# Kernel optimization log

Hardware: AMD Instinct MI355X
Metric: run time of the kernel (lower is better)

The kernel has to match this reference:

```python
import jax, jax.numpy as jnp
import numpy as np

NEG_INF = -9e15  # matches torch's -9000000000000000.0 mask fill
LEAKY_SLOPE = 0.01  # F.leaky_relu default


def setup_inputs() -> dict:
    key = jax.random.key(0)
    ks = jax.random.split(key, 6)
    B, N, F_in, F_out = 4, 4096, 256, 128
    h = jax.random.normal(ks[0], (B, N, F_in), dtype=jnp.float32)
    adj = jax.random.randint(ks[1], (B, N, N), 0, 2, dtype=jnp.int32)
    W_w = jax.random.normal(ks[2], (F_out, F_in), dtype=jnp.float32) * (1.0 / np.sqrt(F_in))
    W_b = jax.random.normal(ks[3], (F_out,), dtype=jnp.float32) * 0.01
    a_w = jax.random.normal(ks[4], (2 * F_out,), dtype=jnp.float32) * (1.0 / np.sqrt(2 * F_out))
    a_b = jax.random.normal(ks[5], (), dtype=jnp.float32) * 0.01
    return {"h": h, "adj": adj, "W_w": W_w, "W_b": W_b, "a_w": a_w, "a_b": a_b}


def reference(h, adj, W_w, W_b, a_w, a_b):
    # Wh: [B, N, F_out]
    Wh = jnp.einsum('bnf,of->bno', h, W_w) + W_b
    F_out = Wh.shape[-1]
    # a([Wh_i, Wh_j]) decomposes as a_src.Wh_i + a_dst.Wh_j + a_b (linearity),
    # avoiding the O(N^2 * 2F) repeat+cat intermediate while computing identical math.
    a_src, a_dst = a_w[:F_out], a_w[F_out:]
    src = jnp.einsum('bno,o->bn', Wh, a_src)  # [B, N]
    dst = jnp.einsum('bno,o->bn', Wh, a_dst)  # [B, N]
    e = src[:, :, None] + dst[:, None, :] + a_b  # [B, N, N]
    e = jnp.where(e >= 0, e, LEAKY_SLOPE * e)  # leaky_relu
    masked = jnp.where(adj > 0, e, NEG_INF)
    attention = jax.nn.softmax(masked, axis=-1)  # row softmax over neighbors j
    h_prime = jnp.einsum('bij,bjo->bio', attention, Wh)
    return h_prime
```

## Files before the change

### kernel.cpp

```cpp
#include <hip/hip_runtime.h>
#include <hip/hip_bf16.h>

typedef __attribute__((ext_vector_type(4))) float f32x4;
typedef __attribute__((ext_vector_type(8))) short s16x8;
typedef unsigned long long u64;

#define NB_ 4
#define N_ 4096
#define FI_ 256
#define FO_ 128
#define NROWS 16384
#define SPLIT 4
#define JSTEP 32
#define NSTEPS ((N_ / SPLIT) / JSTEP)

__device__ __forceinline__ unsigned pkbf(float a, float b) {
    __hip_bfloat162 t = __float22bfloat162_rn(make_float2(a, b));
    unsigned r; __builtin_memcpy(&r, &t, 4); return r;
}

typedef __attribute__((address_space(1))) const void CGV;
typedef __attribute__((address_space(3))) void LDSV;
__device__ __forceinline__ void gload16(const void* g, void* l) {
    __builtin_amdgcn_global_load_lds((CGV*)g, (LDSV*)l, 16, 0, 0);
}

__global__ __launch_bounds__(256) void k0_packw(
    const float* __restrict__ Ww, __hip_bfloat16* __restrict__ whi,
    __hip_bfloat16* __restrict__ wlo)
{
    int idx = blockIdx.x * 256 + threadIdx.x;
    float v = Ww[idx];
    __hip_bfloat16 hi = __float2bfloat16(v);
    whi[idx] = hi;
    wlo[idx] = __float2bfloat16(v - __bfloat162float(hi));
}

__global__ __launch_bounds__(256) void k1_wh(
    const float* __restrict__ h, const __hip_bfloat16* __restrict__ whi,
    const __hip_bfloat16* __restrict__ wlo, const float* __restrict__ Wb,
    const float* __restrict__ aw, const float* __restrict__ ab,
    __hip_bfloat16* __restrict__ WhT, float* __restrict__ srcv,
    float* __restrict__ dstbv, unsigned* __restrict__ auxp)
{
    __shared__ float lds[16][132];
    const int tid = threadIdx.x;
    const int w = tid >> 6, l = tid & 63;
    const int lr = l & 15, g = l >> 4;
    const int r0 = blockIdx.x * 16;
    const float* hp = h + (size_t)(r0 + lr) * FI_ + g * 8;

    f32x4 acc[2] = {(f32x4)0.f, (f32x4)0.f};

    #pragma unroll
    for (int kt = 0; kt < 8; ++kt) {
        f32x4 x0 = *(const f32x4*)(hp + kt * 32);
        f32x4 x1 = *(const f32x4*)(hp + kt * 32 + 4);
        float xx[8];
        #pragma unroll
        for (int t = 0; t < 4; ++t) { xx[t] = x0[t]; xx[t + 4] = x1[t]; }
        union { s16x8 v; unsigned u[4]; } ahi, alo;
        #pragma unroll
        for (int t = 0; t < 4; ++t) {
            float a0 = xx[2 * t], a1 = xx[2 * t + 1];
            unsigned uh = pkbf(a0, a1);
            ahi.u[t] = uh;
            float h0f = __uint_as_float(uh << 16);
            float h1f = __uint_as_float(uh & 0xffff0000u);
            alo.u[t] = pkbf(a0 - h0f, a1 - h1f);
        }
        #pragma unroll
        for (int c = 0; c < 2; ++c) {
            const int o = w * 32 + c * 16 + lr;
            s16x8 bh = *(const s16x8*)(whi + (size_t)o * FI_ + kt * 32 + g * 8);
            s16x8 bl = *(const s16x8*)(wlo + (size_t)o * FI_ + kt * 32 + g * 8);
            acc[c] = __builtin_amdgcn_mfma_f32_16x16x32_bf16(ahi.v, bh, acc[c], 0, 0, 0);
            acc[c] = __builtin_amdgcn_mfma_f32_16x16x32_bf16(alo.v, bh, acc[c], 0, 0, 0);
            acc[c] = __builtin_amdgcn_mfma_f32_16x16x32_bf16(ahi.v, bl, acc[c], 0, 0, 0);
        }
    }

    #pragma unroll
    for (int c = 0; c < 2; ++c) {
        int col = w * 32 + c * 16 + lr;
        float wb = Wb[col];
        #pragma unroll
        for (int kk = 0; kk < 4; ++kk)
            lds[g * 4 + kk][col] = acc[c][kk] + wb;
    }
    __syncthreads();

    {
        const int o = tid >> 1, half = tid & 1;
        const int bb = r0 >> 12, nn = (r0 & 4095) + half * 8;
        union { s16x8 v; unsigned u[4]; } af;
        #pragma unroll
        for (int i = 0; i < 4; ++i)
            af.u[i] = pkbf(lds[half * 8 + 2 * i][o], lds[half * 8 + 2 * i + 1][o]);
        *(s16x8*)(WhT + ((size_t)bb * FO_ + o) * N_ + nn) = af.v;
    }

    {
        const int row = tid >> 4, seg = tid & 15;
        float sp = 0.f, dp = 0.f;
        #pragma unroll
        for (int i = 0; i < 8; ++i) {
            float v = lds[row][seg * 8 + i];
            sp += v * aw[seg * 8 + i];
            dp += v * aw[FO_ + seg * 8 + i];
        }
        #pragma unroll
        for (int off = 8; off >= 1; off >>= 1) {
            sp += __shfl_xor(sp, off);
            dp += __shfl_xor(dp, off);
        }
        if (seg == 0) {
            int r = r0 + row;
            srcv[r] = sp;
            float db = dp + ab[0];
            dstbv[r] = db;
            auxp[r] = pkbf(__expf(db), __expf(0.01f * db));
        }
    }
}

__global__ __launch_bounds__(256) void k2b_max(
    const float* __restrict__ dstbv, float* __restrict__ maxv)
{
    const int b = blockIdx.x;
    const int t = threadIdx.x, w = t >> 6, l = t & 63;
    float m = -3.4e38f;
    for (int i = t; i < N_; i += 256) m = fmaxf(m, dstbv[b * N_ + i]);
    #pragma unroll
    for (int off = 32; off >= 1; off >>= 1) m = fmaxf(m, __shfl_xor(m, off));
    __shared__ float red[4];
    if (l == 0) red[w] = m;
    __syncthreads();
    if (t == 0) maxv[b] = fmaxf(fmaxf(red[0], red[1]), fmaxf(red[2], red[3]));
}

__global__ __launch_bounds__(256, 4) void k3_gat(
    const int* __restrict__ adj, const __hip_bfloat16* __restrict__ WhT,
    const float* __restrict__ srcv, const unsigned* __restrict__ auxp,
    const float* __restrict__ maxv, float* __restrict__ pacc,
    float* __restrict__ prow)
{
    __shared__ __hip_bfloat16 bbuf[2][4096];
    __shared__ float rsum[64];

    const int t = threadIdx.x;
    const int w = t >> 6, l = t & 63;
    const int lr = l & 15, g = l >> 4;
    const int b = blockIdx.x >> 6;
    const int rbase = (blockIdx.x & 63) * 64 + w * 16;
    const int myrow = rbase + lr;
    const int j0 = blockIdx.y * (N_ / SPLIT);

    float C1, C2;
    {
        float s = srcv[b * N_ + myrow];
        float eub = s + maxv[b];
        float m = fmaxf(eub, 0.01f * eub);
        C1 = __expf(s - m);
        C2 = __expf(0.01f * s - m);
    }

    const int* adjp = adj + ((size_t)(b * N_ + myrow)) * N_ + j0 + g * 8;
    const unsigned* axp = auxp + (size_t)b * N_ + j0 + g * 8;
    const short* wsrc = (const short*)WhT +
                        ((size_t)b * FO_ + (w & 3) * 16 + lr) * N_ + j0 + g * 8;

    f32x4 acc[8];
    #pragma unroll
    for (int ot = 0; ot < 8; ++ot) acc[ot] = (f32x4)0.f;
    float rs = 0.f;

    auto stage = [&](int bi, int s) {
        const int jb = s * JSTEP;
        gload16(wsrc + (size_t)((0 * 4) * 16) * N_ + jb, &bbuf[bi][(0 * 256 + w * 64) * 8]);
        gload16(wsrc + (size_t)((1 * 4) * 16) * N_ + jb, &bbuf[bi][(1 * 256 + w * 64) * 8]);
    };

    int4 a0c, a1c; uint4 xc0, xc1;
    stage(0, 0);
    a0c = *(const int4*)(adjp);
    a1c = *(const int4*)(adjp + 4);
    xc0 = *(const uint4*)(axp);
    xc1 = *(const uint4*)(axp + 4);
    __syncthreads();
    int cur = 0;

    for (int s = 0; s < NSTEPS; ++s) {
        int4 a0n = {0,0,0,0}, a1n = {0,0,0,0};
        uint4 xn0 = {0,0,0,0}, xn1 = {0,0,0,0};
        if (s + 1 < NSTEPS) {
            stage(cur ^ 1, s + 1);
            const int jn = (s + 1) * JSTEP;
            a0n = *(const int4*)(adjp + jn);
            a1n = *(const int4*)(adjp + jn + 4);
            xn0 = *(const uint4*)(axp + jn);
            xn1 = *(const uint4*)(axp + jn + 4);
        }

        const unsigned ax[8] = {xc0.x, xc0.y, xc0.z, xc0.w, xc1.x, xc1.y, xc1.z, xc1.w};
        const int av[8] = {a0c.x, a0c.y, a0c.z, a0c.w, a1c.x, a1c.y, a1c.z, a1c.w};
        float p[8];
        #pragma unroll
        for (int e = 0; e < 8; ++e) {
            float e1f = __uint_as_float(ax[e] << 16);
            float e2f = __uint_as_float(ax[e] & 0xffff0000u);
            float v = fmaxf(e1f * C1, e2f * C2);
            p[e] = (av[e] > 0) ? v : 0.f;
            rs += p[e];
        }
        union { s16x8 v; unsigned u[4]; } af;
        af.u[0] = pkbf(p[0], p[1]); af.u[1] = pkbf(p[2], p[3]);
        af.u[2] = pkbf(p[4], p[5]); af.u[3] = pkbf(p[6], p[7]);

        #pragma unroll
        for (int ot = 0; ot < 8; ++ot) {
            s16x8 Bf = *(const s16x8*)&bbuf[cur][(ot * 64 + l) * 8];
            acc[ot] = __builtin_amdgcn_mfma_f32_16x16x32_bf16(af.v, Bf, acc[ot], 0, 0, 0);
        }

        __syncthreads();
        a0c = a0n; a1c = a1n; xc0 = xn0; xc1 = xn1;
        cur ^= 1;
    }

    rs += __shfl_xor(rs, 16);
    rs += __shfl_xor(rs, 32);
    if (g == 0) rsum[w * 16 + lr] = rs;
    __syncthreads();

    const size_t sb = (size_t)blockIdx.y * ((size_t)NROWS * FO_);
    #pragma unroll
    for (int kk = 0; kk < 4; ++kk) {
        int grow = b * N_ + rbase + g * 4 + kk;
        float* pp = pacc + sb + (size_t)grow * FO_ + lr;
        #pragma unroll
        for (int ot = 0; ot < 8; ++ot)
            pp[ot * 16] = acc[ot][kk];
        if (lr == 0)
            prow[blockIdx.y * NROWS + grow] = rsum[w * 16 + g * 4 + kk];
    }
}

__global__ __launch_bounds__(256) void k4_comb(
    const float* __restrict__ pacc, const float* __restrict__ prow,
    float* __restrict__ out)
{
    const int idx = blockIdx.x * 256 + threadIdx.x;
    const int grow = idx >> 7;
    float s = 0.f, rs = 0.f;
    #pragma unroll
    for (int si = 0; si < SPLIT; ++si) {
        s  += pacc[(size_t)si * ((size_t)NROWS * FO_) + idx];
        rs += prow[si * NROWS + grow];
    }
    out[idx] = s / rs;
}

extern "C" void kernel_launch(void* const* d_in, const int* in_sizes, int n_in,
                              void* d_out, int out_size, void* d_ws, size_t ws_size,
                              hipStream_t stream)
{
    const float* h  = (const float*)d_in[0];
    const int* adj  = (const int*)d_in[1];
    const float* Ww = (const float*)d_in[2];
    const float* Wb = (const float*)d_in[3];
    const float* aw = (const float*)d_in[4];
    const float* ab = (const float*)d_in[5];
    float* out = (float*)d_out;

    char* wsb = (char*)d_ws;
    float* pacc          = (float*)wsb;
    __hip_bfloat16* WhT  = (__hip_bfloat16*)(wsb + 33554432u);
    char* aux            = wsb + 37748736u;
    float* srcv          = (float*)(aux);
    float* dstbv         = (float*)(aux + (64u << 10));
    unsigned* auxp       = (unsigned*)(aux + (128u << 10));
    __hip_bfloat16* whi  = (__hip_bfloat16*)(aux + (192u << 10));
    __hip_bfloat16* wlo  = (__hip_bfloat16*)(aux + (256u << 10));
    float* maxv          = (float*)(aux + (320u << 10));
    float* prow          = (float*)(aux + (384u << 10));

    k0_packw<<<128, 256, 0, stream>>>(Ww, whi, wlo);
    k1_wh<<<1024, 256, 0, stream>>>(h, whi, wlo, Wb, aw, ab, WhT, srcv, dstbv, auxp);
    k2b_max<<<4, 256, 0, stream>>>(dstbv, maxv);
    dim3 g3(NB_ * 64, SPLIT);
    k3_gat<<<g3, 256, 0, stream>>>(adj, WhT, srcv, auxp, maxv, pacc, prow);
    k4_comb<<<8192, 256, 0, stream>>>(pacc, prow, out);
}
```

Measured before the change: 144.6 us.

## Stage adjacency via swizzled LDS and pre-tile Wh into MFMA fragment layout

k1 now writes Wh in a pre-tiled fragment-ordered layout so each 32-column j-step of k3 is one contiguous 8KB chunk loaded with coalesced global_load_lds. k3 now streams the adjacency tile through double-buffered LDS using an XOR swizzle, instead of per-lane direct register loads. Each wave now computes 2 row tiles by 4 output tiles rather than 1 by 8, reusing the B fragments across row tiles. The aim is better coalescing and latency hiding on the adj stream, which dominates memory traffic. The cost is extra LDS use, which may affect occupancy.

```diff
diff --git a/kernel.cpp b/kernel.cpp
--- a/kernel.cpp
+++ b/kernel.cpp
@@ -11,8 +11,7 @@
 #define FO_ 128
 #define NROWS 16384
 #define SPLIT 4
-#define JSTEP 32
-#define NSTEPS ((N_ / SPLIT) / JSTEP)
+#define NSTEPS ((N_ / SPLIT) / 32)
 
 __device__ __forceinline__ unsigned pkbf(float a, float b) {
     __hip_bfloat162 t = __float22bfloat162_rn(make_float2(a, b));
@@ -40,7 +39,7 @@
     const float* __restrict__ h, const __hip_bfloat16* __restrict__ whi,
     const __hip_bfloat16* __restrict__ wlo, const float* __restrict__ Wb,
     const float* __restrict__ aw, const float* __restrict__ ab,
-    __hip_bfloat16* __restrict__ WhT, float* __restrict__ srcv,
+    short* __restrict__ WhTf, float* __restrict__ srcv,
     float* __restrict__ dstbv, unsigned* __restrict__ auxp)
 {
     __shared__ float lds[16][132];
@@ -91,13 +90,17 @@
     __syncthreads();
 
     {
-        const int o = tid >> 1, half = tid & 1;
-        const int bb = r0 >> 12, nn = (r0 & 4095) + half * 8;
+        const int o = tid >> 1, joct = tid & 1;
+        const int jblk = (r0 & 4095) >> 5;
+        const int bb = r0 >> 12;
+        const int lb = ((r0 >> 3) & 3) + joct;
         union { s16x8 v; unsigned u[4]; } af;
         #pragma unroll
-        for (int i = 0; i < 4; ++i)
-            af.u[i] = pkbf(lds[half * 8 + 2 * i][o], lds[half * 8 + 2 * i + 1][o]);
-        *(s16x8*)(WhT + ((size_t)bb * FO_ + o) * N_ + nn) = af.v;
+        for (int q = 0; q < 4; ++q)
+            af.u[q] = pkbf(lds[joct * 8 + 2 * q][o], lds[joct * 8 + 2 * q + 1][o]);
+        short* dst = WhTf + (((size_t)bb * 128 + jblk) * 8 + (o >> 4)) * 512
+                          + ((o & 15) + 16 * lb) * 8;
+        *(s16x8*)dst = af.v;
     }
 
     {
@@ -140,109 +143,148 @@
 }
 
 __global__ __launch_bounds__(256, 4) void k3_gat(
-    const int* __restrict__ adj, const __hip_bfloat16* __restrict__ WhT,
+    const int* __restrict__ adj, const short* __restrict__ WhTf,
     const float* __restrict__ srcv, const unsigned* __restrict__ auxp,
     const float* __restrict__ maxv, float* __restrict__ pacc,
     float* __restrict__ prow)
 {
-    __shared__ __hip_bfloat16 bbuf[2][4096];
+    __shared__ int adjb[2][64][32];
+    __shared__ __hip_bfloat16 whb[2][4096];
     __shared__ float rsum[64];
 
     const int t = threadIdx.x;
     const int w = t >> 6, l = t & 63;
     const int lr = l & 15, g = l >> 4;
+    const int rh = w & 1, oh = w >> 1;
     const int b = blockIdx.x >> 6;
-    const int rbase = (blockIdx.x & 63) * 64 + w * 16;
-    const int myrow = rbase + lr;
+    const int rblk = (blockIdx.x & 63) * 64;
+    const int bN = b * N_;
     const int j0 = blockIdx.y * (N_ / SPLIT);
 
-    float C1, C2;
+    float C1[2], C2[2];
     {
-        float s = srcv[b * N_ + myrow];
-        float eub = s + maxv[b];
-        float m = fmaxf(eub, 0.01f * eub);
-        C1 = __expf(s - m);
-        C2 = __expf(0.01f * s - m);
-    }
-
-    const int* adjp = adj + ((size_t)(b * N_ + myrow)) * N_ + j0 + g * 8;
-    const unsigned* axp = auxp + (size_t)b * N_ + j0 + g * 8;
-    const short* wsrc = (const short*)WhT +
-                        ((size_t)b * FO_ + (w & 3) * 16 + lr) * N_ + j0 + g * 8;
-
-    f32x4 acc[8];
-    #pragma unroll
-    for (int ot = 0; ot < 8; ++ot) acc[ot] = (f32x4)0.f;
-    float rs = 0.f;
-
-    auto stage = [&](int bi, int s) {
-        const int jb = s * JSTEP;
-        gload16(wsrc + (size_t)((0 * 4) * 16) * N_ + jb, &bbuf[bi][(0 * 256 + w * 64) * 8]);
-        gload16(wsrc + (size_t)((1 * 4) * 16) * N_ + jb, &bbuf[bi][(1 * 256 + w * 64) * 8]);
+        const float mdb = maxv[b];
+        #pragma unroll
+        for (int rt = 0; rt < 2; ++rt) {
+            int r = rblk + rh * 32 + rt * 16 + lr;
+            float s = srcv[bN + r];
+            float eub = s + mdb;
+            float m = fmaxf(eub, 0.01f * eub);
+            C1[rt] = __expf(s - m);
+            C2[rt] = __expf(0.01f * s - m);
+        }
+    }
+
+    const unsigned* axp = auxp + (size_t)bN + j0 + g * 8;
+    const short* whsrc = WhTf + ((size_t)b * 128 + (j0 >> 5)) * 4096;
+
+    f32x4 acc[2][4];
+    #pragma unroll
+    for (int rt = 0; rt < 2; ++rt)
+        #pragma unroll
+        for (int ot = 0; ot < 4; ++ot) acc[rt][ot] = (f32x4)0.f;
+    float rs0 = 0.f, rs1 = 0.f;
+
+    auto stage_adj = [&](int bi, int s) {
+        const int jb = j0 + s * 32;
+        #pragma unroll
+        for (int i = 0; i < 2; ++i) {
+            int r = (t >> 3) + i * 32;
+            int c = t & 7;
+            const int* src = adj + (size_t)(bN + rblk + r) * N_ + jb
+                                 + ((c ^ (r & 7)) << 2);
+            gload16(src, &adjb[bi][0][0] + (size_t)(i * 256 + w * 64) * 4);
+        }
     };
-
-    int4 a0c, a1c; uint4 xc0, xc1;
-    stage(0, 0);
-    a0c = *(const int4*)(adjp);
-    a1c = *(const int4*)(adjp + 4);
+    auto stage_wh = [&](int bi, int s) {
+        const short* src = whsrc + (size_t)s * 4096;
+        #pragma unroll
+        for (int i = 0; i < 2; ++i)
+            gload16(src + (size_t)(i * 256 + t) * 8,
+                    &whb[bi][0] + (size_t)(i * 256 + w * 64) * 8);
+    };
+
+    uint4 xc0, xc1;
+    stage_adj(0, 0);
+    stage_wh(0, 0);
     xc0 = *(const uint4*)(axp);
     xc1 = *(const uint4*)(axp + 4);
     __syncthreads();
     int cur = 0;
 
     for (int s = 0; s < NSTEPS; ++s) {
-        int4 a0n = {0,0,0,0}, a1n = {0,0,0,0};
-        uint4 xn0 = {0,0,0,0}, xn1 = {0,0,0,0};
-        if (s + 1 < NSTEPS) {
-            stage(cur ^ 1, s + 1);
-            const int jn = (s + 1) * JSTEP;
-            a0n = *(const int4*)(adjp + jn);
-            a1n = *(const int4*)(adjp + jn + 4);
+        uint4 xn0 = {0, 0, 0, 0}, xn1 = {0, 0, 0, 0};
+        const bool more = (s + 1 < NSTEPS);
+        if (more) {
+            stage_adj(cur ^ 1, s + 1);
+            stage_wh(cur ^ 1, s + 1);
+            const int jn = (s + 1) * 32;
             xn0 = *(const uint4*)(axp + jn);
             xn1 = *(const uint4*)(axp + jn + 4);
         }
 
-        const unsigned ax[8] = {xc0.x, xc0.y, xc0.z, xc0.w, xc1.x, xc1.y, xc1.z, xc1.w};
-        const int av[8] = {a0c.x, a0c.y, a0c.z, a0c.w, a1c.x, a1c.y, a1c.z, a1c.w};
-        float p[8];
+        const unsigned ax[8] = {xc0.x, xc0.y, xc0.z, xc0.w,
+                                xc1.x, xc1.y, xc1.z, xc1.w};
+        float e1f[8], e2f[8];
         #pragma unroll
         for (int e = 0; e < 8; ++e) {
-            float e1f = __uint_as_float(ax[e] << 16);
-            float e2f = __uint_as_float(ax[e] & 0xffff0000u);
-            float v = fmaxf(e1f * C1, e2f * C2);
-            p[e] = (av[e] > 0) ? v : 0.f;
-            rs += p[e];
-        }
-        union { s16x8 v; unsigned u[4]; } af;
-        af.u[0] = pkbf(p[0], p[1]); af.u[1] = pkbf(p[2], p[3]);
-        af.u[2] = pkbf(p[4], p[5]); af.u[3] = pkbf(p[6], p[7]);
-
-        #pragma unroll
-        for (int ot = 0; ot < 8; ++ot) {
-            s16x8 Bf = *(const s16x8*)&bbuf[cur][(ot * 64 + l) * 8];
-            acc[ot] = __builtin_amdgcn_mfma_f32_16x16x32_bf16(af.v, Bf, acc[ot], 0, 0, 0);
+            e1f[e] = __uint_as_float(ax[e] << 16);
+            e2f[e] = __uint_as_float(ax[e] & 0xffff0000u);
+        }
+        s16x8 Bf[4];
+        #pragma unroll
+        for (int ot = 0; ot < 4; ++ot)
+            Bf[ot] = *(const s16x8*)&whb[cur][(size_t)((oh * 4 + ot) * 64 + l) * 8];
+
+        #pragma unroll
+        for (int rt = 0; rt < 2; ++rt) {
+            const int R = rh * 32 + rt * 16 + lr;
+            const int4 a0 = *(const int4*)&adjb[cur][R][((2 * g) ^ (lr & 7)) << 2];
+            const int4 a1 = *(const int4*)&adjb[cur][R][((2 * g + 1) ^ (lr & 7)) << 2];
+            const int av[8] = {a0.x, a0.y, a0.z, a0.w, a1.x, a1.y, a1.z, a1.w};
+            float p[8];
+            #pragma unroll
+            for (int e = 0; e < 8; ++e) {
+                float v = fmaxf(e1f[e] * C1[rt], e2f[e] * C2[rt]);
+                p[e] = (av[e] > 0) ? v : 0.f;
+                if (rt == 0) rs0 += p[e]; else rs1 += p[e];
+            }
+            union { s16x8 v; unsigned u[4]; } af;
+            af.u[0] = pkbf(p[0], p[1]); af.u[1] = pkbf(p[2], p[3]);
+            af.u[2] = pkbf(p[4], p[5]); af.u[3] = pkbf(p[6], p[7]);
+            #pragma unroll
+            for (int ot = 0; ot < 4; ++ot)
+                acc[rt][ot] = __builtin_amdgcn_mfma_f32_16x16x32_bf16(
+                    af.v, Bf[ot], acc[rt][ot], 0, 0, 0);
         }
 
         __syncthreads();
-        a0c = a0n; a1c = a1n; xc0 = xn0; xc1 = xn1;
+        xc0 = xn0; xc1 = xn1;
         cur ^= 1;
     }
 
-    rs += __shfl_xor(rs, 16);
-    rs += __shfl_xor(rs, 32);
-    if (g == 0) rsum[w * 16 + lr] = rs;
+    rs0 += __shfl_xor(rs0, 16); rs0 += __shfl_xor(rs0, 32);
+    rs1 += __shfl_xor(rs1, 16); rs1 += __shfl_xor(rs1, 32);
+    if (oh == 0 && l < 16) {
+        rsum[rh * 32 + l] = rs0;
+        rsum[rh * 32 + 16 + l] = rs1;
+    }
     __syncthreads();
 
     const size_t sb = (size_t)blockIdx.y * ((size_t)NROWS * FO_);
     #pragma unroll
-    for (int kk = 0; kk < 4; ++kk) {
-        int grow = b * N_ + rbase + g * 4 + kk;
-        float* pp = pacc + sb + (size_t)grow * FO_ + lr;
-        #pragma unroll
-        for (int ot = 0; ot < 8; ++ot)
-            pp[ot * 16] = acc[ot][kk];
-        if (lr == 0)
-            prow[blockIdx.y * NROWS + grow] = rsum[w * 16 + g * 4 + kk];
+    for (int rt = 0; rt < 2; ++rt) {
+        #pragma unroll
+        for (int kk = 0; kk < 4; ++kk) {
+            int rloc = rh * 32 + rt * 16 + g * 4 + kk;
+            int grow = bN + rblk + rloc;
+            float* pp = pacc + sb + (size_t)grow * FO_ + oh * 64 + lr;
+            #pragma unroll
+            for (int ot = 0; ot < 4; ++ot)
+                pp[ot * 16] = acc[rt][ot][kk];
+            if (oh == 0 && lr == 0)
+                prow[blockIdx.y * NROWS + grow] = rsum[rloc];
+        }
     }
 }
 
@@ -275,7 +317,7 @@
 
     char* wsb = (char*)d_ws;
     float* pacc          = (float*)wsb;
-    __hip_bfloat16* WhT  = (__hip_bfloat16*)(wsb + 33554432u);
+    short* WhTf          = (short*)(wsb + 33554432u);
     char* aux            = wsb + 37748736u;
     float* srcv          = (float*)(aux);
     float* dstbv         = (float*)(aux + (64u << 10));
@@ -286,9 +328,9 @@
     float* prow          = (float*)(aux + (384u << 10));
 
     k0_packw<<<128, 256, 0, stream>>>(Ww, whi, wlo);
-    k1_wh<<<1024, 256, 0, stream>>>(h, whi, wlo, Wb, aw, ab, WhT, srcv, dstbv, auxp);
+    k1_wh<<<1024, 256, 0, stream>>>(h, whi, wlo, Wb, aw, ab, WhTf, srcv, dstbv, auxp);
     k2b_max<<<4, 256, 0, stream>>>(dstbv, maxv);
     dim3 g3(NB_ * 64, SPLIT);
-    k3_gat<<<g3, 256, 0, stream>>>(adj, WhT, srcv, auxp, maxv, pacc, prow);
+    k3_gat<<<g3, 256, 0, stream>>>(adj, WhTf, srcv, auxp, maxv, pacc, prow);
     k4_comb<<<8192, 256, 0, stream>>>(pacc, prow, out);
 }
```

New measurement: 130.8 us. 1.11x faster.
